# Kernel tuning notes

Measured on AMD Instinct MI355X. Metric: run time of the kernel, lower is better.

The kernel has to match this reference:

```python
import jax, jax.numpy as jnp
import numpy as np

N, D, H, O = 512, 128, 256, 256

def setup_inputs() -> dict:
    key = jax.random.key(0)
    ks = jax.random.split(key, 10)
    s = lambda fan_in: 1.0 / np.sqrt(fan_in)
    return {
        "x": jax.random.normal(ks[0], (N, D), dtype=jnp.float32),
        "adj": jax.random.uniform(ks[1], (N, N), dtype=jnp.float32),
        # mpnn_compute: MLP(2D -> H -> H)
        "W1": jax.random.normal(ks[2], (H, 2 * D), dtype=jnp.float32) * s(2 * D),
        "b1": jnp.zeros((H,), dtype=jnp.float32),
        "W2": jax.random.normal(ks[3], (H, H), dtype=jnp.float32) * s(H),
        "b2": jnp.zeros((H,), dtype=jnp.float32),
        # out_compute: MLP(H -> H -> O)
        "Wo1": jax.random.normal(ks[4], (H, H), dtype=jnp.float32) * s(H),
        "bo1": jnp.zeros((H,), dtype=jnp.float32),
        "Wo2": jax.random.normal(ks[5], (O, H), dtype=jnp.float32) * s(H),
        "bo2": jnp.zeros((O,), dtype=jnp.float32),
    }


def reference(x, adj, W1, b1, W2, b2, Wo1, bo1, Wo2, bo2):
    n, d = x.shape
    # e[i, j] = concat(x[j], x[i]); split W1 so we never materialize the cat:
    # linear_1(e)[i,j] = x[j] @ Wa^T + x[i] @ Wb^T + b1
    Wa = W1[:, :d]   # acts on x[j] (first half of cat = x1 = x broadcast over i)
    Wb = W1[:, d:]   # acts on x[i] (second half = x2)
    pa = x @ Wa.T    # [N, H], indexed by j
    pb = x @ Wb.T    # [N, H], indexed by i
    h = jax.nn.relu(pa[None, :, :] + pb[:, None, :] + b1)  # [N, N, H]
    e = jnp.einsum('ijh,kh->ijk', h, W2) + b2               # [N, N, H]
    pred = jnp.mean(adj[:, :, None] * e, axis=1)            # [N, H]
    # out_compute MLP (normalize_input=False)
    h2 = jax.nn.relu(pred @ Wo1.T + bo1)
    return h2 @ Wo2.T + bo2                                  # [N, O]
```

## Files before the change

### kernel.cpp

```cpp
#include <hip/hip_runtime.h>

#define NN 512
#define DD 128
#define HH 256

typedef unsigned int uint32;
typedef unsigned short u16;

__device__ __forceinline__ uint32 bfr(float f) {
    uint32 u = __float_as_uint(f);
    return (u + 0x7fffu + ((u >> 16) & 1u)) >> 16;
}

__global__ __launch_bounds__(256) void k0_tr(const float* __restrict__ W1,
                                             const float* __restrict__ W2,
                                             const float* __restrict__ Wo1,
                                             const float* __restrict__ Wo2,
                                             float* __restrict__ W1T,
                                             u16* __restrict__ wTb) {
    __shared__ float tl[64][68];
    const int b = blockIdx.x;
    const int t = threadIdx.x;
    const int m = b >> 4, tile = b & 15;
    const float* src = (m == 0) ? W1 : (m == 1) ? W2 : (m == 2) ? Wo1 : Wo2;
    const int sr0 = (tile >> 2) * 64;
    const int sc0 = (tile & 3) * 64;
    const int rr = t >> 4;
    const int cc = (t & 15) * 4;
    #pragma unroll
    for (int it = 0; it < 4; ++it) {
        const int row = rr + 16 * it;
        float4 v = *(const float4*)&src[(sr0 + row) * HH + sc0 + cc];
        tl[row][cc + 0] = v.x;
        tl[row][cc + 1] = v.y;
        tl[row][cc + 2] = v.z;
        tl[row][cc + 3] = v.w;
    }
    __syncthreads();
    if (m == 0) {
        #pragma unroll
        for (int it = 0; it < 4; ++it) {
            const int lc = rr + 16 * it;
            float4 o;
            o.x = tl[cc + 0][lc];
            o.y = tl[cc + 1][lc];
            o.z = tl[cc + 2][lc];
            o.w = tl[cc + 3][lc];
            *(float4*)&W1T[(sc0 + lc) * HH + sr0 + cc] = o;
        }
    } else {
        u16* dst = wTb + (m - 1) * (HH * HH);
        #pragma unroll
        for (int it = 0; it < 4; ++it) {
            const int lc = rr + 16 * it;
            uint32 lo = bfr(tl[cc + 0][lc]) | (bfr(tl[cc + 1][lc]) << 16);
            uint32 hi = bfr(tl[cc + 2][lc]) | (bfr(tl[cc + 3][lc]) << 16);
            uint32* p = (uint32*)&dst[(sc0 + lc) * HH + sr0 + cc];
            p[0] = lo;
            p[1] = hi;
        }
    }
}

__global__ __launch_bounds__(256) void k1_papb(const float* __restrict__ x,
                                               const float* __restrict__ W1T,
                                               const float* __restrict__ b1,
                                               float* __restrict__ pa,
                                               float* __restrict__ pbb) {
    __shared__ float xs[2][DD];
    const int b = blockIdx.x;
    const int t = threadIdx.x;
    const int i0 = b * 2;
    if (t < 64) {
        const int f = t * 4;
        *(float4*)&xs[f >> 7][f & 127] = *(const float4*)&x[i0 * DD + f];
    }
    __syncthreads();
    const float* wt = W1T + t;
    const int crot = (b * 8) & 127;
    float pe0 = 0.f, po0 = 0.f, pe1 = 0.f, po1 = 0.f;
    float qe0 = 0.f, qo0 = 0.f, qe1 = 0.f, qo1 = 0.f;
    #pragma unroll 2
    for (int cc0 = 0; cc0 < 128; cc0 += 8) {
        const int c = (cc0 + crot) & 127;
        float w0 = wt[(c + 0) * HH], w1 = wt[(c + 1) * HH];
        float w2 = wt[(c + 2) * HH], w3 = wt[(c + 3) * HH];
        float w4 = wt[(c + 4) * HH], w5 = wt[(c + 5) * HH];
        float w6 = wt[(c + 6) * HH], w7 = wt[(c + 7) * HH];
        float v0 = wt[(128 + c + 0) * HH], v1 = wt[(128 + c + 1) * HH];
        float v2 = wt[(128 + c + 2) * HH], v3 = wt[(128 + c + 3) * HH];
        float v4 = wt[(128 + c + 4) * HH], v5 = wt[(128 + c + 5) * HH];
        float v6 = wt[(128 + c + 6) * HH], v7 = wt[(128 + c + 7) * HH];
        float4 x0a = *(const float4*)&xs[0][c];
        float4 x0b = *(const float4*)&xs[0][c + 4];
        float4 x1a = *(const float4*)&xs[1][c];
        float4 x1b = *(const float4*)&xs[1][c + 4];
        pe0 += w0 * x0a.x + w1 * x0a.y + w2 * x0a.z + w3 * x0a.w;
        po0 += w4 * x0b.x + w5 * x0b.y + w6 * x0b.z + w7 * x0b.w;
        pe1 += w0 * x1a.x + w1 * x1a.y + w2 * x1a.z + w3 * x1a.w;
        po1 += w4 * x1b.x + w5 * x1b.y + w6 * x1b.z + w7 * x1b.w;
        qe0 += v0 * x0a.x + v1 * x0a.y + v2 * x0a.z + v3 * x0a.w;
        qo0 += v4 * x0b.x + v5 * x0b.y + v6 * x0b.z + v7 * x0b.w;
        qe1 += v0 * x1a.x + v1 * x1a.y + v2 * x1a.z + v3 * x1a.w;
        qo1 += v4 * x1b.x + v5 * x1b.y + v6 * x1b.z + v7 * x1b.w;
    }
    const float bb = b1[t];
    pa[i0 * HH + t] = pe0 + po0;
    pa[(i0 + 1) * HH + t] = pe1 + po1;
    pbb[i0 * HH + t] = qe0 + qo0 + bb;
    pbb[(i0 + 1) * HH + t] = qe1 + qo1 + bb;
}

__global__ __launch_bounds__(1024) void k2_rest(const float* __restrict__ adj,
                                                const float* __restrict__ pa,
                                                const float* __restrict__ pbb,
                                                const u16* __restrict__ wTb,
                                                const float* __restrict__ b2,
                                                const float* __restrict__ bo1,
                                                const float* __restrict__ bo2,
                                                float* __restrict__ out) {
    __shared__ float adjs[2][NN];
    __shared__ float4 pbbs4[2][64];
    __shared__ float ts[2][HH];
    __shared__ float buf1[2][HH];
    __shared__ float buf2[2][HH];
    __shared__ float redbuf[8192];
    __shared__ float rsum_s[2];

    const int b = blockIdx.x;
    const int t = threadIdx.x;
    const int i0 = b * 2;

    if (t < 256) {
        const int f = t * 4;
        *(float4*)&adjs[f >> 9][f & 511] = *(const float4*)&adj[(i0 + (f >> 9)) * NN + (f & 511)];
    } else if (t < 384) {
        const int u = t - 256;
        const int r = u >> 6, q = u & 63;
        pbbs4[r][q] = *(const float4*)&pbb[(i0 + r) * HH + q * 4];
    }
    __syncthreads();

    if (t < 128) {
        const int r = t >> 6, l = t & 63;
        float s = 0.f;
        #pragma unroll
        for (int m = 0; m < 8; ++m) s += adjs[r][l + 64 * m];
        #pragma unroll
        for (int off = 32; off > 0; off >>= 1) s += __shfl_down(s, off, 64);
        if (l == 0) rsum_s[r] = s;
    }

    {
        const int hq = t & 63;
        const int js = t >> 6;
        const float4 pb0 = pbbs4[0][hq];
        const float4 pb1 = pbbs4[1][hq];
        float4 ac0 = {0.f, 0.f, 0.f, 0.f};
        float4 ac1 = {0.f, 0.f, 0.f, 0.f};
        #pragma unroll 4
        for (int jj = 0; jj < 32; ++jj) {
            const int j = js * 32 + ((jj + b) & 31);
            float4 p = *(const float4*)&pa[j * HH + hq * 4];
            const float a0 = adjs[0][j];
            const float a1 = adjs[1][j];
            ac0.x += a0 * fmaxf(p.x + pb0.x, 0.f);
            ac0.y += a0 * fmaxf(p.y + pb0.y, 0.f);
            ac0.z += a0 * fmaxf(p.z + pb0.z, 0.f);
            ac0.w += a0 * fmaxf(p.w + pb0.w, 0.f);
            ac1.x += a1 * fmaxf(p.x + pb1.x, 0.f);
            ac1.y += a1 * fmaxf(p.y + pb1.y, 0.f);
            ac1.z += a1 * fmaxf(p.z + pb1.z, 0.f);
            ac1.w += a1 * fmaxf(p.w + pb1.w, 0.f);
        }
        *(float4*)&redbuf[(js * 2 + 0) * 256 + hq * 4] = ac0;
        *(float4*)&redbuf[(js * 2 + 1) * 256 + hq * 4] = ac1;
        __syncthreads();
        if (t < 512) {
            const int r = t >> 8, h = t & 255;
            float s = 0.f;
            #pragma unroll
            for (int q = 0; q < 16; ++q) s += redbuf[(q * 2 + r) * 256 + h];
            ts[r][h] = s;
        }
    }
    __syncthreads();

    const int kq = t & 63;
    const int hp = t >> 6;
    const uint32* W2U  = (const uint32*)wTb;
    const uint32* Wo1U = W2U + (HH * HH) / 2;
    const uint32* Wo2U = W2U + (HH * HH);

    {
        float4 a0 = {0.f, 0.f, 0.f, 0.f};
        float4 a1 = {0.f, 0.f, 0.f, 0.f};
        #pragma unroll 4
        for (int hh = 0; hh < 16; ++hh) {
            const int h = hp * 16 + hh;
            uint32 wx = W2U[h * 128 + kq * 2];
            uint32 wy = W2U[h * 128 + kq * 2 + 1];
            float w0 = __uint_as_float(wx << 16);
            float w1 = __uint_as_float(wx & 0xffff0000u);
            float w2 = __uint_as_float(wy << 16);
            float w3 = __uint_as_float(wy & 0xffff0000u);
            const float v0 = ts[0][h];
            const float v1 = ts[1][h];
            a0.x += w0 * v0; a0.y += w1 * v0; a0.z += w2 * v0; a0.w += w3 * v0;
            a1.x += w0 * v1; a1.y += w1 * v1; a1.z += w2 * v1; a1.w += w3 * v1;
        }
        *(float4*)&redbuf[(hp * 2 + 0) * 256 + kq * 4] = a0;
        *(float4*)&redbuf[(hp * 2 + 1) * 256 + kq * 4] = a1;
        __syncthreads();
        if (t < 512) {
            const int r = t >> 8, k = t & 255;
            float s = 0.f;
            #pragma unroll
            for (int p = 0; p < 16; ++p) s += redbuf[(p * 2 + r) * 256 + k];
            buf1[r][k] = (s + b2[k] * rsum_s[r]) * (1.0f / (float)NN);
        }
    }
    __syncthreads();

    {
        float4 a0 = {0.f, 0.f, 0.f, 0.f};
        float4 a1 = {0.f, 0.f, 0.f, 0.f};
        #pragma unroll 4
        for (int hh = 0; hh < 16; ++hh) {
            const int h = hp * 16 + hh;
            uint32 wx = Wo1U[h * 128 + kq * 2];
            uint32 wy = Wo1U[h * 128 + kq * 2 + 1];
            float w0 = __uint_as_float(wx << 16);
            float w1 = __uint_as_float(wx & 0xffff0000u);
            float w2 = __uint_as_float(wy << 16);
            float w3 = __uint_as_float(wy & 0xffff0000u);
            const float v0 = buf1[0][h];
            const float v1 = buf1[1][h];
            a0.x += w0 * v0; a0.y += w1 * v0; a0.z += w2 * v0; a0.w += w3 * v0;
            a1.x += w0 * v1; a1.y += w1 * v1; a1.z += w2 * v1; a1.w += w3 * v1;
        }
        *(float4*)&redbuf[(hp * 2 + 0) * 256 + kq * 4] = a0;
        *(float4*)&redbuf[(hp * 2 + 1) * 256 + kq * 4] = a1;
        __syncthreads();
        if (t < 512) {
            const int r = t >> 8, k = t & 255;
            float s = 0.f;
            #pragma unroll
            for (int p = 0; p < 16; ++p) s += redbuf[(p * 2 + r) * 256 + k];
            buf2[r][k] = fmaxf(s + bo1[k], 0.f);
        }
    }
    __syncthreads();

    {
        float4 a0 = {0.f, 0.f, 0.f, 0.f};
        float4 a1 = {0.f, 0.f, 0.f, 0.f};
        #pragma unroll 4
        for (int hh = 0; hh < 16; ++hh) {
            const int h = hp * 16 + hh;
            uint32 wx = Wo2U[h * 128 + kq * 2];
            uint32 wy = Wo2U[h * 128 + kq * 2 + 1];
            float w0 = __uint_as_float(wx << 16);
            float w1 = __uint_as_float(wx & 0xffff0000u);
            float w2 = __uint_as_float(wy << 16);
            float w3 = __uint_as_float(wy & 0xffff0000u);
            const float v0 = buf2[0][h];
            const float v1 = buf2[1][h];
            a0.x += w0 * v0; a0.y += w1 * v0; a0.z += w2 * v0; a0.w += w3 * v0;
            a1.x += w0 * v1; a1.y += w1 * v1; a1.z += w2 * v1; a1.w += w3 * v1;
        }
        *(float4*)&redbuf[(hp * 2 + 0) * 256 + kq * 4] = a0;
        *(float4*)&redbuf[(hp * 2 + 1) * 256 + kq * 4] = a1;
        __syncthreads();
        if (t < 512) {
            const int r = t >> 8, k = t & 255;
            float s = 0.f;
            #pragma unroll
            for (int p = 0; p < 16; ++p) s += redbuf[(p * 2 + r) * 256 + k];
            out[(i0 + r) * HH + k] = s + bo2[k];
        }
    }
}

extern "C" void kernel_launch(void* const* d_in, const int* in_sizes, int n_in,
                              void* d_out, int out_size, void* d_ws, size_t ws_size,
                              hipStream_t stream) {
    const float* x   = (const float*)d_in[0];
    const float* adj = (const float*)d_in[1];
    const float* W1  = (const float*)d_in[2];
    const float* b1  = (const float*)d_in[3];
    const float* W2  = (const float*)d_in[4];
    const float* b2  = (const float*)d_in[5];
    const float* Wo1 = (const float*)d_in[6];
    const float* bo1 = (const float*)d_in[7];
    const float* Wo2 = (const float*)d_in[8];
    const float* bo2 = (const float*)d_in[9];
    float* out = (float*)d_out;
    float* ws  = (float*)d_ws;

    float* W1T = ws;
    u16*   wTb = (u16*)(ws + 65536);
    float* pa  = ws + 163840;
    float* pbb = ws + 294912;

    k0_tr<<<64, 256, 0, stream>>>(W1, W2, Wo1, Wo2, W1T, wTb);
    k1_papb<<<256, 256, 0, stream>>>(x, W1T, b1, pa, pbb);
    k2_rest<<<256, 1024, 0, stream>>>(adj, pa, pbb, wTb, b2, bo1, bo2, out);
}
```

Before: 30.77 us.

## Split aggregation into separate kernel with 4-row tiles and bf16 pa

Measured after the change: 45.97 us. 49.4% more time.

```diff
diff --git a/kernel.cpp b/kernel.cpp
--- a/kernel.cpp
+++ b/kernel.cpp
@@ -65,7 +65,7 @@
 __global__ __launch_bounds__(256) void k1_papb(const float* __restrict__ x,
                                                const float* __restrict__ W1T,
                                                const float* __restrict__ b1,
-                                               float* __restrict__ pa,
+                                               u16* __restrict__ pa_bf,
                                                float* __restrict__ pbb) {
     __shared__ float xs[2][DD];
     const int b = blockIdx.x;
@@ -105,22 +105,90 @@
         qo1 += v4 * x1b.x + v5 * x1b.y + v6 * x1b.z + v7 * x1b.w;
     }
     const float bb = b1[t];
-    pa[i0 * HH + t] = pe0 + po0;
-    pa[(i0 + 1) * HH + t] = pe1 + po1;
+    pa_bf[i0 * HH + t] = (u16)bfr(pe0 + po0);
+    pa_bf[(i0 + 1) * HH + t] = (u16)bfr(pe1 + po1);
     pbb[i0 * HH + t] = qe0 + qo0 + bb;
     pbb[(i0 + 1) * HH + t] = qe1 + qo1 + bb;
 }
 
-__global__ __launch_bounds__(1024) void k2_rest(const float* __restrict__ adj,
-                                                const float* __restrict__ pa,
-                                                const float* __restrict__ pbb,
-                                                const u16* __restrict__ wTb,
-                                                const float* __restrict__ b2,
-                                                const float* __restrict__ bo1,
-                                                const float* __restrict__ bo2,
-                                                float* __restrict__ out) {
-    __shared__ float adjs[2][NN];
-    __shared__ float4 pbbs4[2][64];
+__global__ __launch_bounds__(512) void kT(const float* __restrict__ adj,
+                                          const u16* __restrict__ pa_bf,
+                                          const float* __restrict__ pbb,
+                                          float* __restrict__ Tsum,
+                                          float* __restrict__ rowsum) {
+    __shared__ float smem[6144];
+    float* adjs = smem;
+    float2* red2 = (float2*)(smem + 2048);
+
+    const int b = blockIdx.x;
+    const int t = threadIdx.x;
+    const int itile = b & 127;
+    const int half = b >> 7;
+    const int i0 = itile * 4;
+
+    {
+        const int f = t * 4;
+        const int r = f >> 9;
+        const int c = f & 511;
+        *(float4*)&adjs[r * 512 + c] = *(const float4*)&adj[(i0 + r) * NN + c];
+    }
+    const int jg = t >> 6;
+    const int hu = t & 63;
+    float2 pbv[4];
+    #pragma unroll
+    for (int r = 0; r < 4; ++r)
+        pbv[r] = *(const float2*)&pbb[(i0 + r) * HH + half * 128 + hu * 2];
+    float2 acc[4] = {{0.f, 0.f}, {0.f, 0.f}, {0.f, 0.f}, {0.f, 0.f}};
+    __syncthreads();
+
+    const uint32* paU = (const uint32*)pa_bf;
+    const int colU = half * 64 + hu;
+    #pragma unroll 4
+    for (int jj = 0; jj < 64; ++jj) {
+        const int j = jg * 64 + jj;
+        uint32 w = paU[j * 128 + colU];
+        float p0 = __uint_as_float(w << 16);
+        float p1 = __uint_as_float(w & 0xffff0000u);
+        #pragma unroll
+        for (int r = 0; r < 4; ++r) {
+            const float a = adjs[r * 512 + j];
+            acc[r].x += a * fmaxf(p0 + pbv[r].x, 0.f);
+            acc[r].y += a * fmaxf(p1 + pbv[r].y, 0.f);
+        }
+    }
+    #pragma unroll
+    for (int r = 0; r < 4; ++r) red2[(jg * 4 + r) * 64 + hu] = acc[r];
+    __syncthreads();
+
+    {
+        const int r = t >> 7;
+        const int hl = t & 127;
+        const float* redf = (const float*)red2;
+        float s = 0.f;
+        #pragma unroll
+        for (int g = 0; g < 8; ++g)
+            s += redf[((g * 4 + r) * 64 + (hl >> 1)) * 2 + (hl & 1)];
+        Tsum[(i0 + r) * HH + half * 128 + hl] = s;
+    }
+
+    if (half == 0 && t < 256) {
+        const int r = t >> 6, l = t & 63;
+        float s = 0.f;
+        #pragma unroll
+        for (int m = 0; m < 8; ++m) s += adjs[r * 512 + l + 64 * m];
+        #pragma unroll
+        for (int off = 32; off > 0; off >>= 1) s += __shfl_down(s, off, 64);
+        if (l == 0) rowsum[i0 + r] = s;
+    }
+}
+
+__global__ __launch_bounds__(1024) void kS(const float* __restrict__ Tsum,
+                                           const float* __restrict__ rowsum,
+                                           const u16* __restrict__ wTb,
+                                           const float* __restrict__ b2,
+                                           const float* __restrict__ bo1,
+                                           const float* __restrict__ bo2,
+                                           float* __restrict__ out) {
     __shared__ float ts[2][HH];
     __shared__ float buf1[2][HH];
     __shared__ float buf2[2][HH];
@@ -131,58 +199,12 @@
     const int t = threadIdx.x;
     const int i0 = b * 2;
 
-    if (t < 256) {
+    if (t < 128) {
         const int f = t * 4;
-        *(float4*)&adjs[f >> 9][f & 511] = *(const float4*)&adj[(i0 + (f >> 9)) * NN + (f & 511)];
-    } else if (t < 384) {
-        const int u = t - 256;
-        const int r = u >> 6, q = u & 63;
-        pbbs4[r][q] = *(const float4*)&pbb[(i0 + r) * HH + q * 4];
-    }
-    __syncthreads();
-
-    if (t < 128) {
-        const int r = t >> 6, l = t & 63;
-        float s = 0.f;
-        #pragma unroll
-        for (int m = 0; m < 8; ++m) s += adjs[r][l + 64 * m];
-        #pragma unroll
-        for (int off = 32; off > 0; off >>= 1) s += __shfl_down(s, off, 64);
-        if (l == 0) rsum_s[r] = s;
-    }
-
-    {
-        const int hq = t & 63;
-        const int js = t >> 6;
-        const float4 pb0 = pbbs4[0][hq];
-        const float4 pb1 = pbbs4[1][hq];
-        float4 ac0 = {0.f, 0.f, 0.f, 0.f};
-        float4 ac1 = {0.f, 0.f, 0.f, 0.f};
-        #pragma unroll 4
-        for (int jj = 0; jj < 32; ++jj) {
-            const int j = js * 32 + ((jj + b) & 31);
-            float4 p = *(const float4*)&pa[j * HH + hq * 4];
-            const float a0 = adjs[0][j];
-            const float a1 = adjs[1][j];
-            ac0.x += a0 * fmaxf(p.x + pb0.x, 0.f);
-            ac0.y += a0 * fmaxf(p.y + pb0.y, 0.f);
-            ac0.z += a0 * fmaxf(p.z + pb0.z, 0.f);
-            ac0.w += a0 * fmaxf(p.w + pb0.w, 0.f);
-            ac1.x += a1 * fmaxf(p.x + pb1.x, 0.f);
-            ac1.y += a1 * fmaxf(p.y + pb1.y, 0.f);
-            ac1.z += a1 * fmaxf(p.z + pb1.z, 0.f);
-            ac1.w += a1 * fmaxf(p.w + pb1.w, 0.f);
-        }
-        *(float4*)&redbuf[(js * 2 + 0) * 256 + hq * 4] = ac0;
-        *(float4*)&redbuf[(js * 2 + 1) * 256 + hq * 4] = ac1;
-        __syncthreads();
-        if (t < 512) {
-            const int r = t >> 8, h = t & 255;
-            float s = 0.f;
-            #pragma unroll
-            for (int q = 0; q < 16; ++q) s += redbuf[(q * 2 + r) * 256 + h];
-            ts[r][h] = s;
-        }
+        const int r = f >> 8, c = f & 255;
+        *(float4*)&ts[r][c] = *(const float4*)&Tsum[(i0 + r) * HH + c];
+    } else if (t < 130) {
+        rsum_s[t - 128] = rowsum[i0 + (t - 128)];
     }
     __syncthreads();
 
@@ -298,12 +320,15 @@
     float* out = (float*)d_out;
     float* ws  = (float*)d_ws;
 
-    float* W1T = ws;
-    u16*   wTb = (u16*)(ws + 65536);
-    float* pa  = ws + 163840;
-    float* pbb = ws + 294912;
+    float* W1T    = ws;
+    u16*   wTb    = (u16*)(ws + 65536);
+    u16*   pa_bf  = (u16*)(ws + 163840);
+    float* pbb    = ws + 229376;
+    float* Tsum   = ws + 360448;
+    float* rowsum = ws + 491520;
 
     k0_tr<<<64, 256, 0, stream>>>(W1, W2, Wo1, Wo2, W1T, wTb);
-    k1_papb<<<256, 256, 0, stream>>>(x, W1T, b1, pa, pbb);
-    k2_rest<<<256, 1024, 0, stream>>>(adj, pa, pbb, wTb, b2, bo1, bo2, out);
-}
+    k1_papb<<<256, 256, 0, stream>>>(x, W1T, b1, pa_bf, pbb);
+    kT<<<256, 512, 0, stream>>>(adj, pa_bf, pbb, Tsum, rowsum);
+    kS<<<256, 1024, 0, stream>>>(Tsum, rowsum, wTb, b2, bo1, bo2, out);
+}
```

## Fuse weight transpose and pa/pb projection into one launch reading W1 directly

Applied to the files above, without the earlier changes.

Measured after the change: 33.96 us. 1.1x slower.

```diff
diff --git a/kernel.cpp b/kernel.cpp
--- a/kernel.cpp
+++ b/kernel.cpp
@@ -7,49 +7,76 @@
 typedef unsigned int uint32;
 typedef unsigned short u16;
 
+__device__ __forceinline__ float dot4(float4 a, float4 b) {
+    return a.x * b.x + a.y * b.y + a.z * b.z + a.w * b.w;
+}
+
 __device__ __forceinline__ uint32 bfr(float f) {
     uint32 u = __float_as_uint(f);
     return (u + 0x7fffu + ((u >> 16) & 1u)) >> 16;
 }
 
-__global__ __launch_bounds__(256) void k0_tr(const float* __restrict__ W1,
-                                             const float* __restrict__ W2,
-                                             const float* __restrict__ Wo1,
-                                             const float* __restrict__ Wo2,
-                                             float* __restrict__ W1T,
-                                             u16* __restrict__ wTb) {
-    __shared__ float tl[64][68];
+__global__ __launch_bounds__(256) void kA(const float* __restrict__ x,
+                                          const float* __restrict__ W1,
+                                          const float* __restrict__ b1,
+                                          const float* __restrict__ W2,
+                                          const float* __restrict__ Wo1,
+                                          const float* __restrict__ Wo2,
+                                          float* __restrict__ pa,
+                                          float* __restrict__ pbb,
+                                          u16* __restrict__ wTb) {
+    __shared__ float smem[64 * 68];
     const int b = blockIdx.x;
     const int t = threadIdx.x;
-    const int m = b >> 4, tile = b & 15;
-    const float* src = (m == 0) ? W1 : (m == 1) ? W2 : (m == 2) ? Wo1 : Wo2;
-    const int sr0 = (tile >> 2) * 64;
-    const int sc0 = (tile & 3) * 64;
-    const int rr = t >> 4;
-    const int cc = (t & 15) * 4;
-    #pragma unroll
-    for (int it = 0; it < 4; ++it) {
-        const int row = rr + 16 * it;
-        float4 v = *(const float4*)&src[(sr0 + row) * HH + sc0 + cc];
-        tl[row][cc + 0] = v.x;
-        tl[row][cc + 1] = v.y;
-        tl[row][cc + 2] = v.z;
-        tl[row][cc + 3] = v.w;
-    }
-    __syncthreads();
-    if (m == 0) {
+    if (b < 256) {
+        float (*xs)[DD] = (float(*)[DD])smem;
+        const int i0 = b * 2;
+        if (t < 64) {
+            const int f = t * 4;
+            *(float4*)&xs[f >> 7][f & 127] = *(const float4*)&x[i0 * DD + f];
+        }
+        __syncthreads();
+        const int h = t;
+        const float4* w4 = (const float4*)(W1 + h * (2 * DD));
+        const float4* x0 = (const float4*)&xs[0][0];
+        const float4* x1 = (const float4*)&xs[1][0];
+        float a0 = 0.f, a1 = 0.f, c0 = 0.f, c1 = 0.f;
+        #pragma unroll 8
+        for (int d4 = 0; d4 < DD / 4; ++d4) {
+            float4 wa = w4[d4];
+            float4 wb = w4[d4 + 32];
+            float4 v0 = x0[d4];
+            float4 v1 = x1[d4];
+            a0 += dot4(wa, v0);
+            a1 += dot4(wa, v1);
+            c0 += dot4(wb, v0);
+            c1 += dot4(wb, v1);
+        }
+        const float bb = b1[h];
+        pa[i0 * HH + h] = a0;
+        pa[(i0 + 1) * HH + h] = a1;
+        pbb[i0 * HH + h] = c0 + bb;
+        pbb[(i0 + 1) * HH + h] = c1 + bb;
+    } else {
+        float (*tl)[68] = (float(*)[68])smem;
+        const int bb = b - 256;
+        const int m = bb >> 4, tile = bb & 15;
+        const float* src = (m == 0) ? W2 : (m == 1) ? Wo1 : Wo2;
+        u16* dst = wTb + m * (HH * HH);
+        const int sr0 = (tile >> 2) * 64;
+        const int sc0 = (tile & 3) * 64;
+        const int rr = t >> 4;
+        const int cc = (t & 15) * 4;
         #pragma unroll
         for (int it = 0; it < 4; ++it) {
-            const int lc = rr + 16 * it;
-            float4 o;
-            o.x = tl[cc + 0][lc];
-            o.y = tl[cc + 1][lc];
-            o.z = tl[cc + 2][lc];
-            o.w = tl[cc + 3][lc];
-            *(float4*)&W1T[(sc0 + lc) * HH + sr0 + cc] = o;
-        }
-    } else {
-        u16* dst = wTb + (m - 1) * (HH * HH);
+            const int row = rr + 16 * it;
+            float4 v = *(const float4*)&src[(sr0 + row) * HH + sc0 + cc];
+            tl[row][cc + 0] = v.x;
+            tl[row][cc + 1] = v.y;
+            tl[row][cc + 2] = v.z;
+            tl[row][cc + 3] = v.w;
+        }
+        __syncthreads();
         #pragma unroll
         for (int it = 0; it < 4; ++it) {
             const int lc = rr + 16 * it;
@@ -60,55 +87,6 @@
             p[1] = hi;
         }
     }
-}
-
-__global__ __launch_bounds__(256) void k1_papb(const float* __restrict__ x,
-                                               const float* __restrict__ W1T,
-                                               const float* __restrict__ b1,
-                                               float* __restrict__ pa,
-                                               float* __restrict__ pbb) {
-    __shared__ float xs[2][DD];
-    const int b = blockIdx.x;
-    const int t = threadIdx.x;
-    const int i0 = b * 2;
-    if (t < 64) {
-        const int f = t * 4;
-        *(float4*)&xs[f >> 7][f & 127] = *(const float4*)&x[i0 * DD + f];
-    }
-    __syncthreads();
-    const float* wt = W1T + t;
-    const int crot = (b * 8) & 127;
-    float pe0 = 0.f, po0 = 0.f, pe1 = 0.f, po1 = 0.f;
-    float qe0 = 0.f, qo0 = 0.f, qe1 = 0.f, qo1 = 0.f;
-    #pragma unroll 2
-    for (int cc0 = 0; cc0 < 128; cc0 += 8) {
-        const int c = (cc0 + crot) & 127;
-        float w0 = wt[(c + 0) * HH], w1 = wt[(c + 1) * HH];
-        float w2 = wt[(c + 2) * HH], w3 = wt[(c + 3) * HH];
-        float w4 = wt[(c + 4) * HH], w5 = wt[(c + 5) * HH];
-        float w6 = wt[(c + 6) * HH], w7 = wt[(c + 7) * HH];
-        float v0 = wt[(128 + c + 0) * HH], v1 = wt[(128 + c + 1) * HH];
-        float v2 = wt[(128 + c + 2) * HH], v3 = wt[(128 + c + 3) * HH];
-        float v4 = wt[(128 + c + 4) * HH], v5 = wt[(128 + c + 5) * HH];
-        float v6 = wt[(128 + c + 6) * HH], v7 = wt[(128 + c + 7) * HH];
-        float4 x0a = *(const float4*)&xs[0][c];
-        float4 x0b = *(const float4*)&xs[0][c + 4];
-        float4 x1a = *(const float4*)&xs[1][c];
-        float4 x1b = *(const float4*)&xs[1][c + 4];
-        pe0 += w0 * x0a.x + w1 * x0a.y + w2 * x0a.z + w3 * x0a.w;
-        po0 += w4 * x0b.x + w5 * x0b.y + w6 * x0b.z + w7 * x0b.w;
-        pe1 += w0 * x1a.x + w1 * x1a.y + w2 * x1a.z + w3 * x1a.w;
-        po1 += w4 * x1b.x + w5 * x1b.y + w6 * x1b.z + w7 * x1b.w;
-        qe0 += v0 * x0a.x + v1 * x0a.y + v2 * x0a.z + v3 * x0a.w;
-        qo0 += v4 * x0b.x + v5 * x0b.y + v6 * x0b.z + v7 * x0b.w;
-        qe1 += v0 * x1a.x + v1 * x1a.y + v2 * x1a.z + v3 * x1a.w;
-        qo1 += v4 * x1b.x + v5 * x1b.y + v6 * x1b.z + v7 * x1b.w;
-    }
-    const float bb = b1[t];
-    pa[i0 * HH + t] = pe0 + po0;
-    pa[(i0 + 1) * HH + t] = pe1 + po1;
-    pbb[i0 * HH + t] = qe0 + qo0 + bb;
-    pbb[(i0 + 1) * HH + t] = qe1 + qo1 + bb;
 }
 
 __global__ __launch_bounds__(1024) void k2_rest(const float* __restrict__ adj,
@@ -298,12 +276,10 @@
     float* out = (float*)d_out;
     float* ws  = (float*)d_ws;
 
-    float* W1T = ws;
-    u16*   wTb = (u16*)(ws + 65536);
-    float* pa  = ws + 163840;
-    float* pbb = ws + 294912;
-
-    k0_tr<<<64, 256, 0, stream>>>(W1, W2, Wo1, Wo2, W1T, wTb);
-    k1_papb<<<256, 256, 0, stream>>>(x, W1T, b1, pa, pbb);
+    u16*   wTb = (u16*)ws;
+    float* pa  = ws + 98304;
+    float* pbb = ws + 229376;
+
+    kA<<<304, 256, 0, stream>>>(x, W1, b1, W2, Wo1, Wo2, pa, pbb, wTb);
     k2_rest<<<256, 1024, 0, stream>>>(adj, pa, pbb, wTb, b2, bo1, bo2, out);
 }
```
